# Optimization experiments

Hardware: AMD Instinct MI355X
Metric: run time of the kernel (lower is better)

The kernel has to match this reference:

```python
import jax, jax.numpy as jnp
import numpy as np

N = 100000

def gcn_conv(x, src, dst, W, b, n):
    # x: [N, Fin]; src/dst: [E'] (self-loops already included); W: [Fin, Fout]
    h = x @ W  # [N, Fout]
    deg = jax.ops.segment_sum(jnp.ones_like(dst, dtype=h.dtype), dst, num_segments=n)  # [N]
    dinv = deg ** -0.5  # deg >= 1 due to self-loops
    norm = dinv[src] * dinv[dst]  # [E']
    msg = h[src] * norm[:, None]  # gather + scale, [E', Fout]
    out = jax.ops.segment_sum(msg, dst, num_segments=n)  # scatter-add to targets
    return out + b

def setup_inputs() -> dict:
    key = jax.random.key(0)
    k1, k2, k3, k4, k5, k6 = jax.random.split(key, 6)
    x = jax.random.normal(k1, (N, 128), dtype=jnp.float32)
    edge_index = jax.random.randint(k2, (2, 1600000), 0, N, dtype=jnp.int32)
    W1 = jax.random.normal(k3, (128, 64), dtype=jnp.float32) * 0.1
    b1 = jnp.zeros((64,), dtype=jnp.float32)
    W2 = jax.random.normal(k4, (64, 41), dtype=jnp.float32) * 0.1
    b2 = jnp.zeros((41,), dtype=jnp.float32)
    return {"x": x, "edge_index": edge_index, "W1": W1, "b1": b1, "W2": W2, "b2": b2}

def reference(x, edge_index, W1, b1, W2, b2):
    n = x.shape[0]
    loops = jnp.arange(n, dtype=edge_index.dtype)
    src = jnp.concatenate([edge_index[0], loops])  # add self-loops (PyG gcn_norm default)
    dst = jnp.concatenate([edge_index[1], loops])
    # dropout is identity in eval mode (self.training=False)
    h = gcn_conv(x, src, dst, W1, b1, n)
    h = jax.nn.relu(h)
    out = gcn_conv(h, src, dst, W2, b2, n)
    return out
```

## Files before the change

kernel.cpp:

```cpp
#include <hip/hip_runtime.h>


#define FIN 128
#define F1  64
#define F2  41
#define FP  64

#define BSH    8
#define BCAP   6144
#define CHUNK_P 4096

#define MT 128
#define KC 16

#define SMEM_BYTES 24576

__device__ __forceinline__ unsigned short f2bf(float f) {
    unsigned u = __builtin_bit_cast(unsigned, f);
    u += 0x7FFFu + ((u >> 16) & 1u);
    return (unsigned short)(u >> 16);
}
__device__ __forceinline__ float bf2f(unsigned short h) {
    unsigned u = ((unsigned)h) << 16;
    return __builtin_bit_cast(float, u);
}

__global__ __launch_bounds__(256) void k_partmm1(
    const int* __restrict__ src, const int* __restrict__ dst,
    unsigned short* __restrict__ offs, int* __restrict__ pairs,
    int E, int nchunks, int NB,
    const float* __restrict__ x, const float* __restrict__ W1,
    unsigned short* __restrict__ hs, int n) {
    __shared__ alignas(16) char smem[SMEM_BYTES];
    int tid = threadIdx.x;
    if ((int)blockIdx.x < nchunks) {
        int* hist = (int*)smem;
        int* lex  = hist + 512;
        int* limg = lex + 256;
        int e0  = blockIdx.x * CHUNK_P;
        int ds[CHUNK_P / 256], ss[CHUNK_P / 256];
#pragma unroll
        for (int j = 0; j < CHUNK_P / 256; j++) {
            int e = e0 + j * 256 + tid;
            if (e < E) { ds[j] = dst[e]; ss[j] = src[e]; } else ds[j] = -1;
        }
        hist[tid] = 0; hist[tid + 256] = 0;
        __syncthreads();
#pragma unroll
        for (int j = 0; j < CHUNK_P / 256; j++)
            if (ds[j] >= 0) atomicAdd(&hist[ds[j] >> BSH], 1);
        __syncthreads();
        int b0 = 2 * tid, b1 = 2 * tid + 1;
        int c0 = hist[b0], c1 = hist[b1];
        int s  = c0 + c1;
        lex[tid] = s;
        __syncthreads();
        for (int off = 1; off < 256; off <<= 1) {
            int v = lex[tid];
            int a = (tid >= off) ? lex[tid - off] : 0;
            __syncthreads();
            lex[tid] = v + a;
            __syncthreads();
        }
        int incl = lex[tid];
        int ex0 = incl - s;
        int ex1 = ex0 + c0;
        unsigned short* orow = offs + (size_t)blockIdx.x * (NB + 1);
        if (b0 < NB) orow[b0] = (unsigned short)ex0;
        if (b1 < NB) orow[b1] = (unsigned short)ex1;
        if (tid == 255) orow[NB] = (unsigned short)incl;
        hist[b0] = ex0; hist[b1] = ex1;
        __syncthreads();
#pragma unroll
        for (int j = 0; j < CHUNK_P / 256; j++) {
            if (ds[j] >= 0) {
                int b = ds[j] >> BSH;
                int p = atomicAdd(&hist[b], 1);
                limg[p] = (ss[j] << BSH) | (ds[j] & 255);
            }
        }
        __syncthreads();
        int tot = lex[255];
        int* pout = pairs + (size_t)blockIdx.x * CHUNK_P;
        for (int k = tid; k < tot; k += 256)
            pout[k] = limg[k];
    } else {
        unsigned short* Ws = (unsigned short*)smem;
        float (*As)[MT] = (float(*)[MT])(smem + FIN * F1 * 2);
        int n0 = ((int)blockIdx.x - nchunks) * MT;
#pragma unroll
        for (int j = 0; j < 8; j++) {
            int f = j * 256 + tid;
            float4 w4 = ((const float4*)W1)[f];
            ushort4 o = { f2bf(w4.x), f2bf(w4.y), f2bf(w4.z), f2bf(w4.w) };
            ((ushort4*)Ws)[f] = o;
        }
        int m0 = (tid & 15) * 8;
        int c0 = (tid >> 4) * 4;
        int m_l = tid & 127;
        int kh  = (tid >> 7) * 8;
        bool mvalid = (n0 + m_l) < n;
        const float* xrow = x + (size_t)(n0 + m_l) * FIN + kh;
        float acc[8][4] = {};
        for (int kc = 0; kc < FIN; kc += KC) {
            __syncthreads();
            float4 v0 = mvalid ? *(const float4*)(xrow + kc)     : float4{0.f,0.f,0.f,0.f};
            float4 v1 = mvalid ? *(const float4*)(xrow + kc + 4) : float4{0.f,0.f,0.f,0.f};
            As[kh + 0][m_l] = v0.x; As[kh + 1][m_l] = v0.y;
            As[kh + 2][m_l] = v0.z; As[kh + 3][m_l] = v0.w;
            As[kh + 4][m_l] = v1.x; As[kh + 5][m_l] = v1.y;
            As[kh + 6][m_l] = v1.z; As[kh + 7][m_l] = v1.w;
            __syncthreads();
#pragma unroll
            for (int k = 0; k < KC; k++) {
                float4 a0 = *(const float4*)&As[k][m0];
                float4 a1 = *(const float4*)&As[k][m0 + 4];
                ushort4 wq = *(const ushort4*)&Ws[(kc + k) * F1 + c0];
                float wx = bf2f(wq.x), wy = bf2f(wq.y);
                float wz = bf2f(wq.z), ww = bf2f(wq.w);
                float a[8] = {a0.x, a0.y, a0.z, a0.w, a1.x, a1.y, a1.z, a1.w};
#pragma unroll
                for (int i = 0; i < 8; i++) {
                    acc[i][0] += a[i] * wx;
                    acc[i][1] += a[i] * wy;
                    acc[i][2] += a[i] * wz;
                    acc[i][3] += a[i] * ww;
                }
            }
        }
#pragma unroll
        for (int i = 0; i < 8; i++) {
            int node = n0 + m0 + i;
            if (node < n) {
                ushort4 o = { f2bf(acc[i][0]), f2bf(acc[i][1]),
                              f2bf(acc[i][2]), f2bf(acc[i][3]) };
                *(ushort4*)&hs[((size_t)node << 6) + c0] = o;
            }
        }
    }
}

__global__ __launch_bounds__(1024) void k_build(
    const unsigned short* __restrict__ offs, const int* __restrict__ pairs,
    int nchunks, int NB, int* __restrict__ adj,
    int2* __restrict__ rowinfo, float* __restrict__ dinv,
    unsigned short* __restrict__ hs1, int n) {
    __shared__ int lcnt[256];
    __shared__ int lex[256];
    __shared__ int lcur[256];
    __shared__ float ldv[256];
    int tid  = threadIdx.x;
    int wave = tid >> 6;
    int lane = tid & 63;
    int b    = blockIdx.x;
    int NB1  = NB + 1;
    int node0 = b << BSH;
    int base  = b * BCAP;

    if (tid < 256) lcnt[tid] = 0;
    __syncthreads();
    for (int c = wave; c < nchunks; c += 16) {
        int s0 = offs[(size_t)c * NB1 + b];
        int s1 = offs[(size_t)c * NB1 + b + 1];
        const int* pc = pairs + (size_t)c * CHUNK_P;
        for (int i = s0 + lane; i < s1; i += 64)
            atomicAdd(&lcnt[pc[i] & 255], 1);
    }
    __syncthreads();
    int own = (tid < 256) ? lcnt[tid] : 0;
    if (tid < 256) lex[tid] = own;
    __syncthreads();
    for (int off = 1; off < 256; off <<= 1) {
        int val = 0, add = 0;
        if (tid < 256) {
            val = lex[tid];
            add = (tid >= off) ? lex[tid - off] : 0;
        }
        __syncthreads();
        if (tid < 256) lex[tid] = val + add;
        __syncthreads();
    }
    int excl = (tid < 256) ? (lex[tid] - own) : 0;
    float dvn = rsqrtf((float)own + 1.0f);
    if (tid < 256) { lcur[tid] = excl; ldv[tid] = dvn; }
    __syncthreads();
    for (int c = wave; c < nchunks; c += 16) {
        int s0 = offs[(size_t)c * NB1 + b];
        int s1 = offs[(size_t)c * NB1 + b + 1];
        const int* pc = pairs + (size_t)c * CHUNK_P;
        for (int i = s0 + lane; i < s1; i += 64) {
            int pk  = pc[i];
            int pos = atomicAdd(&lcur[pk & 255], 1);
            adj[base + pos] = pk >> BSH;
        }
    }
    int node = node0 + tid;
    if (tid < 256 && node < n) {
        rowinfo[node] = make_int2(base + excl, own);
        dinv[node]    = dvn;
    }
    for (int u = tid; u < 2048; u += 1024) {
        int nd = node0 + (u >> 3);
        if (nd >= n) break;
        float dv = ldv[u >> 3];
        ushort4* p = (ushort4*)&hs1[((size_t)nd << 6) + (u & 7) * 8];
        ushort4 a = p[0], c = p[1];
        a.x = f2bf(bf2f(a.x) * dv); a.y = f2bf(bf2f(a.y) * dv);
        a.z = f2bf(bf2f(a.z) * dv); a.w = f2bf(bf2f(a.w) * dv);
        c.x = f2bf(bf2f(c.x) * dv); c.y = f2bf(bf2f(c.y) * dv);
        c.z = f2bf(bf2f(c.z) * dv); c.w = f2bf(bf2f(c.w) * dv);
        p[0] = a; p[1] = c;
    }
}

__global__ __launch_bounds__(256) void k_agg1mm2(
    const int2* __restrict__ rowinfo, const int* __restrict__ adj,
    const unsigned short* __restrict__ hs, const float* __restrict__ dinv,
    const float* __restrict__ b1, const float* __restrict__ W2,
    unsigned short* __restrict__ hs2, int n, int AT) {
    __shared__ float W2s[F1 * FP];
    __shared__ float H[4][F1];
    int tid  = threadIdx.x;
    int w    = tid >> 6;
    int node = blockIdx.x * 4 + w;
    int lane = tid & 63;
    int grp  = lane >> 4;
    int p4   = (lane & 15) * 4;
    for (int idx = tid; idx < F1 * FP; idx += 256) {
        int k = idx >> 6, c = idx & 63;
        W2s[idx] = (c < F2) ? W2[k * F2 + c] : 0.f;
    }
    if (node < n) {
        int2 ri = rowinfo[node];
        int beg = ri.x, deg = ri.y;
        float4 acc = {0.f, 0.f, 0.f, 0.f};
        if (grp == 0) {
            ushort4 u = *(const ushort4*)&hs[((size_t)node << 6) + p4];
            acc.x = bf2f(u.x); acc.y = bf2f(u.y); acc.z = bf2f(u.z); acc.w = bf2f(u.w);
        }
        for (int base = 0; base < deg; base += 64) {
            int m = deg - base; if (m > 64) m = 64;
            int idx = beg + base + lane;
            int myoff = adj[idx < AT ? idx : 0] << 6;
            int e = 0;
            for (; e + 16 <= m; e += 16) {
                int o0 = __shfl(myoff, e + grp),      o1 = __shfl(myoff, e + 4 + grp);
                int o2 = __shfl(myoff, e + 8 + grp),  o3 = __shfl(myoff, e + 12 + grp);
                ushort4 u0 = *(const ushort4*)&hs[(size_t)o0 + p4];
                ushort4 u1 = *(const ushort4*)&hs[(size_t)o1 + p4];
                ushort4 u2 = *(const ushort4*)&hs[(size_t)o2 + p4];
                ushort4 u3 = *(const ushort4*)&hs[(size_t)o3 + p4];
                acc.x += (bf2f(u0.x) + bf2f(u1.x)) + (bf2f(u2.x) + bf2f(u3.x));
                acc.y += (bf2f(u0.y) + bf2f(u1.y)) + (bf2f(u2.y) + bf2f(u3.y));
                acc.z += (bf2f(u0.z) + bf2f(u1.z)) + (bf2f(u2.z) + bf2f(u3.z));
                acc.w += (bf2f(u0.w) + bf2f(u1.w)) + (bf2f(u2.w) + bf2f(u3.w));
            }
            for (; e < m; e += 4) {
                int sl = e + grp;
                int o = __shfl(myoff, sl);
                if (sl < m) {
                    ushort4 u = *(const ushort4*)&hs[(size_t)o + p4];
                    acc.x += bf2f(u.x); acc.y += bf2f(u.y);
                    acc.z += bf2f(u.z); acc.w += bf2f(u.w);
                }
            }
        }
        acc.x += __shfl_xor(acc.x, 16); acc.y += __shfl_xor(acc.y, 16);
        acc.z += __shfl_xor(acc.z, 16); acc.w += __shfl_xor(acc.w, 16);
        acc.x += __shfl_xor(acc.x, 32); acc.y += __shfl_xor(acc.y, 32);
        acc.z += __shfl_xor(acc.z, 32); acc.w += __shfl_xor(acc.w, 32);
        if (grp == 0) {
            float dvn = dinv[node];
            float4 bg = *(const float4*)&b1[p4];
            float vx = acc.x * dvn + bg.x; vx = vx > 0.f ? vx : 0.f;
            float vy = acc.y * dvn + bg.y; vy = vy > 0.f ? vy : 0.f;
            float vz = acc.z * dvn + bg.z; vz = vz > 0.f ? vz : 0.f;
            float vw = acc.w * dvn + bg.w; vw = vw > 0.f ? vw : 0.f;
            H[w][p4 + 0] = vx; H[w][p4 + 1] = vy;
            H[w][p4 + 2] = vz; H[w][p4 + 3] = vw;
        }
    }
    __syncthreads();
    if (node < n) {
        int c = lane;
        float s = 0.f;
#pragma unroll
        for (int k = 0; k < F1; k += 4) {
            float4 hv = *(const float4*)&H[w][k];
            s += hv.x * W2s[(k + 0) * FP + c];
            s += hv.y * W2s[(k + 1) * FP + c];
            s += hv.z * W2s[(k + 2) * FP + c];
            s += hv.w * W2s[(k + 3) * FP + c];
        }
        hs2[((size_t)node << 6) + c] = f2bf(s * dinv[node]);
    }
}

__global__ __launch_bounds__(256) void k_agg2(
    const int2* __restrict__ rowinfo, const int* __restrict__ adj,
    const unsigned short* __restrict__ hs2, const float* __restrict__ dinv,
    const float* __restrict__ b2, float* __restrict__ out, int n, int AT) {
    int node = blockIdx.x * 4 + (threadIdx.x >> 6);
    if (node >= n) return;
    int lane = threadIdx.x & 63;
    int grp  = lane >> 4;
    int p4   = (lane & 15) * 4;
    int2 ri = rowinfo[node];
    int beg = ri.x, deg = ri.y;
    float4 acc = {0.f, 0.f, 0.f, 0.f};
    if (grp == 0) {
        ushort4 u = *(const ushort4*)&hs2[((size_t)node << 6) + p4];
        acc.x = bf2f(u.x); acc.y = bf2f(u.y); acc.z = bf2f(u.z); acc.w = bf2f(u.w);
    }
    for (int base = 0; base < deg; base += 64) {
        int m = deg - base; if (m > 64) m = 64;
        int idx = beg + base + lane;
        int myoff = adj[idx < AT ? idx : 0] << 6;
        int e = 0;
        for (; e + 16 <= m; e += 16) {
            int o0 = __shfl(myoff, e + grp),      o1 = __shfl(myoff, e + 4 + grp);
            int o2 = __shfl(myoff, e + 8 + grp),  o3 = __shfl(myoff, e + 12 + grp);
            ushort4 u0 = *(const ushort4*)&hs2[(size_t)o0 + p4];
            ushort4 u1 = *(const ushort4*)&hs2[(size_t)o1 + p4];
            ushort4 u2 = *(const ushort4*)&hs2[(size_t)o2 + p4];
            ushort4 u3 = *(const ushort4*)&hs2[(size_t)o3 + p4];
            acc.x += (bf2f(u0.x) + bf2f(u1.x)) + (bf2f(u2.x) + bf2f(u3.x));
            acc.y += (bf2f(u0.y) + bf2f(u1.y)) + (bf2f(u2.y) + bf2f(u3.y));
            acc.z += (bf2f(u0.z) + bf2f(u1.z)) + (bf2f(u2.z) + bf2f(u3.z));
            acc.w += (bf2f(u0.w) + bf2f(u1.w)) + (bf2f(u2.w) + bf2f(u3.w));
        }
        for (; e < m; e += 4) {
            int sl = e + grp;
            int o = __shfl(myoff, sl);
            if (sl < m) {
                ushort4 u = *(const ushort4*)&hs2[(size_t)o + p4];
                acc.x += bf2f(u.x); acc.y += bf2f(u.y);
                acc.z += bf2f(u.z); acc.w += bf2f(u.w);
            }
        }
    }
    acc.x += __shfl_xor(acc.x, 16); acc.y += __shfl_xor(acc.y, 16);
    acc.z += __shfl_xor(acc.z, 16); acc.w += __shfl_xor(acc.w, 16);
    acc.x += __shfl_xor(acc.x, 32); acc.y += __shfl_xor(acc.y, 32);
    acc.z += __shfl_xor(acc.z, 32); acc.w += __shfl_xor(acc.w, 32);
    if (grp == 0) {
        float dv = dinv[node];
        float vv[4] = {acc.x, acc.y, acc.z, acc.w};
#pragma unroll
        for (int j = 0; j < 4; j++) {
            int f = p4 + j;
            if (f < F2) out[(size_t)node * F2 + f] = vv[j] * dv + b2[f];
        }
    }
}

extern "C" void kernel_launch(void* const* d_in, const int* in_sizes, int n_in,
                              void* d_out, int out_size, void* d_ws, size_t ws_size,
                              hipStream_t stream) {
    const float* x  = (const float*)d_in[0];
    const int*   ei = (const int*)d_in[1];
    const float* W1 = (const float*)d_in[2];
    const float* b1 = (const float*)d_in[3];
    const float* W2 = (const float*)d_in[4];
    const float* b2 = (const float*)d_in[5];
    float* out = (float*)d_out;

    const int n = in_sizes[0] / FIN;
    const int E = in_sizes[1] / 2;
    const int* src = ei;
    const int* dst = ei + E;
    const int nbuck   = (n + 255) >> BSH;
    const int nchunks = (E + CHUNK_P - 1) / CHUNK_P;
    const int nmm     = (n + MT - 1) / MT;
    const int nagg    = (n + 3) / 4;
    const int adjtot  = nbuck * BCAP;

    char* ws = (char*)d_ws;
    size_t off = 0;
    auto alloc = [&](size_t bytes) {
        void* p = ws + off;
        off = (off + bytes + 511) & ~(size_t)511;
        return p;
    };
    unsigned short* offs = (unsigned short*)alloc((size_t)nchunks * (nbuck + 1) * 2);
    int*   pairs   = (int*)alloc((size_t)nchunks * CHUNK_P * 4);
    int*   adj     = (int*)alloc((size_t)adjtot * 4 + 256);
    int2*  rowinfo = (int2*)alloc((size_t)n * 8);
    float* dinv    = (float*)alloc((size_t)n * 4);
    unsigned short* hs1 = (unsigned short*)alloc((size_t)n * FP * 2);
    unsigned short* hs2 = (unsigned short*)alloc((size_t)n * FP * 2);

    k_partmm1<<<nchunks + nmm, 256, 0, stream>>>(src, dst, offs, pairs, E, nchunks,
                                                 nbuck, x, W1, hs1, n);
    k_build<<<nbuck, 1024, 0, stream>>>(offs, pairs, nchunks, nbuck, adj, rowinfo,
                                        dinv, hs1, n);
    k_agg1mm2<<<nagg, 256, 0, stream>>>(rowinfo, adj, hs1, dinv, b1, W2, hs2,
                                        n, adjtot);
    k_agg2<<<nagg, 256, 0, stream>>>(rowinfo, adj, hs2, dinv, b2, out, n, adjtot);
}
```

Baseline: 326.8 us.

## Process 64 nodes per block in agg1mm2 and register-tile the W2 matmul

The layer-1 aggregation plus W2 matmul kernel now handles 64 nodes per 512-thread block: each wave aggregates 8 nodes in sequence and stores the ReLU outputs transposed in shared memory. A 4x4 register-tiled matmul on 256 threads then produces hs2. This spreads the per-block W2 load into shared memory over 16x more nodes and gives more FMA reuse per LDS read. In exchange there are fewer, larger blocks, the per-wave aggregation is serialized over 8 nodes, and half the threads sit idle during the matmul.

```diff
diff --git a/kernel.cpp b/kernel.cpp
--- a/kernel.cpp
+++ b/kernel.cpp
@@ -12,6 +12,7 @@
 
 #define MT 128
 #define KC 16
+#define AMT 64
 
 #define SMEM_BYTES 24576
 
@@ -213,86 +214,107 @@
     }
 }
 
-__global__ __launch_bounds__(256) void k_agg1mm2(
+__global__ __launch_bounds__(512) void k_agg1mm2(
     const int2* __restrict__ rowinfo, const int* __restrict__ adj,
     const unsigned short* __restrict__ hs, const float* __restrict__ dinv,
     const float* __restrict__ b1, const float* __restrict__ W2,
     unsigned short* __restrict__ hs2, int n, int AT) {
     __shared__ float W2s[F1 * FP];
-    __shared__ float H[4][F1];
+    __shared__ float Ht[F1][AMT + 4];
     int tid  = threadIdx.x;
     int w    = tid >> 6;
-    int node = blockIdx.x * 4 + w;
     int lane = tid & 63;
     int grp  = lane >> 4;
     int p4   = (lane & 15) * 4;
-    for (int idx = tid; idx < F1 * FP; idx += 256) {
+    int n0   = blockIdx.x * AMT;
+    for (int idx = tid; idx < F1 * FP; idx += 512) {
         int k = idx >> 6, c = idx & 63;
         W2s[idx] = (c < F2) ? W2[k * F2 + c] : 0.f;
     }
-    if (node < n) {
-        int2 ri = rowinfo[node];
-        int beg = ri.x, deg = ri.y;
+    for (int r = 0; r < 8; r++) {
+        int nl   = r * 8 + w;
+        int node = n0 + nl;
         float4 acc = {0.f, 0.f, 0.f, 0.f};
+        if (node < n) {
+            int2 ri = rowinfo[node];
+            int beg = ri.x, deg = ri.y;
+            if (grp == 0) {
+                ushort4 u = *(const ushort4*)&hs[((size_t)node << 6) + p4];
+                acc.x = bf2f(u.x); acc.y = bf2f(u.y);
+                acc.z = bf2f(u.z); acc.w = bf2f(u.w);
+            }
+            for (int base = 0; base < deg; base += 64) {
+                int m = deg - base; if (m > 64) m = 64;
+                int idx = beg + base + lane;
+                int myoff = adj[idx < AT ? idx : 0] << 6;
+                int e = 0;
+                for (; e + 16 <= m; e += 16) {
+                    int o0 = __shfl(myoff, e + grp),      o1 = __shfl(myoff, e + 4 + grp);
+                    int o2 = __shfl(myoff, e + 8 + grp),  o3 = __shfl(myoff, e + 12 + grp);
+                    ushort4 u0 = *(const ushort4*)&hs[(size_t)o0 + p4];
+                    ushort4 u1 = *(const ushort4*)&hs[(size_t)o1 + p4];
+                    ushort4 u2 = *(const ushort4*)&hs[(size_t)o2 + p4];
+                    ushort4 u3 = *(const ushort4*)&hs[(size_t)o3 + p4];
+                    acc.x += (bf2f(u0.x) + bf2f(u1.x)) + (bf2f(u2.x) + bf2f(u3.x));
+                    acc.y += (bf2f(u0.y) + bf2f(u1.y)) + (bf2f(u2.y) + bf2f(u3.y));
+                    acc.z += (bf2f(u0.z) + bf2f(u1.z)) + (bf2f(u2.z) + bf2f(u3.z));
+                    acc.w += (bf2f(u0.w) + bf2f(u1.w)) + (bf2f(u2.w) + bf2f(u3.w));
+                }
+                for (; e < m; e += 4) {
+                    int sl = e + grp;
+                    int o = __shfl(myoff, sl);
+                    if (sl < m) {
+                        ushort4 u = *(const ushort4*)&hs[(size_t)o + p4];
+                        acc.x += bf2f(u.x); acc.y += bf2f(u.y);
+                        acc.z += bf2f(u.z); acc.w += bf2f(u.w);
+                    }
+                }
+            }
+            acc.x += __shfl_xor(acc.x, 16); acc.y += __shfl_xor(acc.y, 16);
+            acc.z += __shfl_xor(acc.z, 16); acc.w += __shfl_xor(acc.w, 16);
+            acc.x += __shfl_xor(acc.x, 32); acc.y += __shfl_xor(acc.y, 32);
+            acc.z += __shfl_xor(acc.z, 32); acc.w += __shfl_xor(acc.w, 32);
+        }
         if (grp == 0) {
-            ushort4 u = *(const ushort4*)&hs[((size_t)node << 6) + p4];
-            acc.x = bf2f(u.x); acc.y = bf2f(u.y); acc.z = bf2f(u.z); acc.w = bf2f(u.w);
-        }
-        for (int base = 0; base < deg; base += 64) {
-            int m = deg - base; if (m > 64) m = 64;
-            int idx = beg + base + lane;
-            int myoff = adj[idx < AT ? idx : 0] << 6;
-            int e = 0;
-            for (; e + 16 <= m; e += 16) {
-                int o0 = __shfl(myoff, e + grp),      o1 = __shfl(myoff, e + 4 + grp);
-                int o2 = __shfl(myoff, e + 8 + grp),  o3 = __shfl(myoff, e + 12 + grp);
-                ushort4 u0 = *(const ushort4*)&hs[(size_t)o0 + p4];
-                ushort4 u1 = *(const ushort4*)&hs[(size_t)o1 + p4];
-                ushort4 u2 = *(const ushort4*)&hs[(size_t)o2 + p4];
-                ushort4 u3 = *(const ushort4*)&hs[(size_t)o3 + p4];
-                acc.x += (bf2f(u0.x) + bf2f(u1.x)) + (bf2f(u2.x) + bf2f(u3.x));
-                acc.y += (bf2f(u0.y) + bf2f(u1.y)) + (bf2f(u2.y) + bf2f(u3.y));
-                acc.z += (bf2f(u0.z) + bf2f(u1.z)) + (bf2f(u2.z) + bf2f(u3.z));
-                acc.w += (bf2f(u0.w) + bf2f(u1.w)) + (bf2f(u2.w) + bf2f(u3.w));
-            }
-            for (; e < m; e += 4) {
-                int sl = e + grp;
-                int o = __shfl(myoff, sl);
-                if (sl < m) {
-                    ushort4 u = *(const ushort4*)&hs[(size_t)o + p4];
-                    acc.x += bf2f(u.x); acc.y += bf2f(u.y);
-                    acc.z += bf2f(u.z); acc.w += bf2f(u.w);
-                }
-            }
-        }
-        acc.x += __shfl_xor(acc.x, 16); acc.y += __shfl_xor(acc.y, 16);
-        acc.z += __shfl_xor(acc.z, 16); acc.w += __shfl_xor(acc.w, 16);
-        acc.x += __shfl_xor(acc.x, 32); acc.y += __shfl_xor(acc.y, 32);
-        acc.z += __shfl_xor(acc.z, 32); acc.w += __shfl_xor(acc.w, 32);
-        if (grp == 0) {
-            float dvn = dinv[node];
-            float4 bg = *(const float4*)&b1[p4];
-            float vx = acc.x * dvn + bg.x; vx = vx > 0.f ? vx : 0.f;
-            float vy = acc.y * dvn + bg.y; vy = vy > 0.f ? vy : 0.f;
-            float vz = acc.z * dvn + bg.z; vz = vz > 0.f ? vz : 0.f;
-            float vw = acc.w * dvn + bg.w; vw = vw > 0.f ? vw : 0.f;
-            H[w][p4 + 0] = vx; H[w][p4 + 1] = vy;
-            H[w][p4 + 2] = vz; H[w][p4 + 3] = vw;
+            float vx = 0.f, vy = 0.f, vz = 0.f, vw = 0.f;
+            if (node < n) {
+                float dvn = dinv[node];
+                float4 bg = *(const float4*)&b1[p4];
+                vx = acc.x * dvn + bg.x; vx = vx > 0.f ? vx : 0.f;
+                vy = acc.y * dvn + bg.y; vy = vy > 0.f ? vy : 0.f;
+                vz = acc.z * dvn + bg.z; vz = vz > 0.f ? vz : 0.f;
+                vw = acc.w * dvn + bg.w; vw = vw > 0.f ? vw : 0.f;
+            }
+            Ht[p4 + 0][nl] = vx; Ht[p4 + 1][nl] = vy;
+            Ht[p4 + 2][nl] = vz; Ht[p4 + 3][nl] = vw;
         }
     }
     __syncthreads();
-    if (node < n) {
-        int c = lane;
-        float s = 0.f;
-#pragma unroll
-        for (int k = 0; k < F1; k += 4) {
-            float4 hv = *(const float4*)&H[w][k];
-            s += hv.x * W2s[(k + 0) * FP + c];
-            s += hv.y * W2s[(k + 1) * FP + c];
-            s += hv.z * W2s[(k + 2) * FP + c];
-            s += hv.w * W2s[(k + 3) * FP + c];
-        }
-        hs2[((size_t)node << 6) + c] = f2bf(s * dinv[node]);
+    if (tid < 256) {
+        int m0 = (tid & 15) * 4;
+        int c0 = (tid >> 4) * 4;
+        float4 r0 = {0.f,0.f,0.f,0.f}, r1 = {0.f,0.f,0.f,0.f};
+        float4 r2 = {0.f,0.f,0.f,0.f}, r3 = {0.f,0.f,0.f,0.f};
+#pragma unroll 4
+        for (int k = 0; k < F1; k++) {
+            float4 av = *(const float4*)&Ht[k][m0];
+            float4 wv = *(const float4*)&W2s[(k << 6) + c0];
+            r0.x += av.x * wv.x; r0.y += av.x * wv.y; r0.z += av.x * wv.z; r0.w += av.x * wv.w;
+            r1.x += av.y * wv.x; r1.y += av.y * wv.y; r1.z += av.y * wv.z; r1.w += av.y * wv.w;
+            r2.x += av.z * wv.x; r2.y += av.z * wv.y; r2.z += av.z * wv.z; r2.w += av.z * wv.w;
+            r3.x += av.w * wv.x; r3.y += av.w * wv.y; r3.z += av.w * wv.z; r3.w += av.w * wv.w;
+        }
+        float4 rr[4] = {r0, r1, r2, r3};
+#pragma unroll
+        for (int i = 0; i < 4; i++) {
+            int node = n0 + m0 + i;
+            if (node < n) {
+                float dv = dinv[node];
+                ushort4 o = { f2bf(rr[i].x * dv), f2bf(rr[i].y * dv),
+                              f2bf(rr[i].z * dv), f2bf(rr[i].w * dv) };
+                *(ushort4*)&hs2[((size_t)node << 6) + c0] = o;
+            }
+        }
     }
 }
 
@@ -372,6 +394,7 @@
     const int nbuck   = (n + 255) >> BSH;
     const int nchunks = (E + CHUNK_P - 1) / CHUNK_P;
     const int nmm     = (n + MT - 1) / MT;
+    const int nagg1   = (n + AMT - 1) / AMT;
     const int nagg    = (n + 3) / 4;
     const int adjtot  = nbuck * BCAP;
 
@@ -394,7 +417,7 @@
                                                  nbuck, x, W1, hs1, n);
     k_build<<<nbuck, 1024, 0, stream>>>(offs, pairs, nchunks, nbuck, adj, rowinfo,
                                         dinv, hs1, n);
-    k_agg1mm2<<<nagg, 256, 0, stream>>>(rowinfo, adj, hs1, dinv, b1, W2, hs2,
-                                        n, adjtot);
+    k_agg1mm2<<<nagg1, 512, 0, stream>>>(rowinfo, adj, hs1, dinv, b1, W2, hs2,
+                                         n, adjtot);
     k_agg2<<<nagg, 256, 0, stream>>>(rowinfo, adj, hs2, dinv, b2, out, n, adjtot);
 }
```

After: 282.3 us, median of 2. 13.6% less time.
